# Optimization experiments

Measured on AMD Instinct MI355X. Metric: run time of the kernel, lower is better.

## Reference

```python
import jax, jax.numpy as jnp
import numpy as np

N = 100000   # nodes
E = 1600000  # edges (avg degree 16)
K = 50       # TAGConv hops per layer


def gcn_norm(edge_index, edge_weight, num_nodes):
    # PyG gcn_norm with add_self_loops=False: D^{-1/2} A D^{-1/2},
    # degree computed at the aggregation (col) side for source_to_target flow.
    row, col = edge_index[0], edge_index[1]
    deg = jax.ops.segment_sum(edge_weight, col, num_segments=num_nodes)
    dis = jnp.where(deg > 0, deg ** -0.5, jnp.zeros_like(deg))
    return dis[row] * edge_weight * dis[col]


def tagconv(x, row, col, norm, W, b):
    # out = sum_{k=0..K} (A_hat^k x) W_k + b, W: [K+1, fin, fout]
    out0 = x @ W[0] + b

    def step(carry, Wk):
        h, acc = carry
        h = jax.ops.segment_sum(norm[:, None] * h[row], col, num_segments=N)
        return (h, acc + h @ Wk), None

    (_, out), _ = jax.lax.scan(step, (x, out0), W[1:])
    return out


def setup_inputs() -> dict:
    key = jax.random.key(0)
    ks = jax.random.split(key, 8)
    edge_index = jax.random.randint(ks[0], (2, E), 0, N)
    edge_weight = jax.random.uniform(ks[1], (E,), dtype=jnp.float32)
    c = jax.random.normal(ks[2], (N,), dtype=jnp.float32)

    def glorot(k, fin, fout):
        lim = (6.0 / (fin + fout)) ** 0.5
        return jax.random.uniform(k, (K + 1, fin, fout), jnp.float32, -lim, lim)

    W1 = glorot(ks[3], 2, 15);  b1 = jnp.zeros((15,), jnp.float32)
    W2 = glorot(ks[4], 15, 30); b2 = jnp.zeros((30,), jnp.float32)
    W3 = glorot(ks[5], 30, 15); b3 = jnp.zeros((15,), jnp.float32)
    W4 = glorot(ks[6], 15, 1);  b4 = jnp.zeros((1,), jnp.float32)
    return {"edge_index": edge_index, "edge_weight": edge_weight, "c": c, "i": 123,
            "W1": W1, "b1": b1, "W2": W2, "b2": b2,
            "W3": W3, "b3": b3, "W4": W4, "b4": b4}


def reference(edge_index, edge_weight, c, i, W1, b1, W2, b2, W3, b3, W4, b4):
    cv = jnp.zeros((N,), jnp.float32).at[i].set(1.0)
    x = jnp.stack([cv, c], axis=1)  # [N, 2]
    row, col = edge_index[0], edge_index[1]
    norm = gcn_norm(edge_index, edge_weight.astype(jnp.float32), N)
    x = jax.nn.relu(tagconv(x, row, col, norm, W1, b1))
    x = jax.nn.relu(tagconv(x, row, col, norm, W2, b2))
    x = jax.nn.relu(tagconv(x, row, col, norm, W3, b3))
    x = jax.nn.relu(tagconv(x, row, col, norm, W4, b4))
    return jnp.squeeze(x)  # [N]
```

## Files before the change

### kernel.cpp

```cpp
#include <hip/hip_runtime.h>

#define NN 100000
#define NE 1600000
#define NB_N ((NN + 255) / 256)
#define NB_E ((NE + 255) / 256)
#define NB_G ((NN + 31) / 32)


__global__ void zero_kernel(int* __restrict__ cnt) {
    int i = blockIdx.x * 256 + threadIdx.x;
    if (i < NN) cnt[i] = 0;
}

__global__ void edge_pass1(const int* __restrict__ ei, int* __restrict__ cnt,
                           int* __restrict__ rank) {
    int e = blockIdx.x * 256 + threadIdx.x;
    if (e < NE) {
        int col = ei[NE + e];
        rank[e] = atomicAdd(&cnt[col], 1);
    }
}

__global__ void scan_block(const int* __restrict__ cnt, int* __restrict__ colptr,
                           int* __restrict__ bsum) {
    __shared__ int s[256];
    int t = threadIdx.x;
    int i = blockIdx.x * 256 + t;
    int v = (i < NN) ? cnt[i] : 0;
    s[t] = v;
    __syncthreads();
    for (int off = 1; off < 256; off <<= 1) {
        int x = (t >= off) ? s[t - off] : 0;
        __syncthreads();
        s[t] += x;
        __syncthreads();
    }
    if (i < NN) colptr[i] = s[t] - v;
    if (t == 255) bsum[blockIdx.x] = s[255];
}

__global__ void scan_top(int* __restrict__ bsum, int nb) {
    __shared__ int s[512];
    int t = threadIdx.x;
    int v = (t < nb) ? bsum[t] : 0;
    s[t] = v;
    __syncthreads();
    for (int off = 1; off < 512; off <<= 1) {
        int x = (t >= off) ? s[t - off] : 0;
        __syncthreads();
        s[t] += x;
        __syncthreads();
    }
    if (t < nb) bsum[t] = s[t] - v;
}

__global__ void scan_add(int* __restrict__ colptr, const int* __restrict__ bsum) {
    int i = blockIdx.x * 256 + threadIdx.x;
    if (i < NN) colptr[i] += bsum[blockIdx.x];
    if (i == 0) colptr[NN] = NE;
}

__global__ void scatter_kernel(const int* __restrict__ ei, const float* __restrict__ ew,
                               const int* __restrict__ colptr, const int* __restrict__ rank,
                               int2* __restrict__ pairs) {
    int e = blockIdx.x * 256 + threadIdx.x;
    if (e < NE) {
        int r = ei[e], col = ei[NE + e];
        pairs[colptr[col] + rank[e]] = make_int2(r, __float_as_int(ew[e]));
    }
}

__global__ void deg_dis_kernel(const int2* __restrict__ pairs, const int* __restrict__ colptr,
                               float* __restrict__ dis) {
    int n = blockIdx.x * 256 + threadIdx.x;
    if (n < NN) {
        int e0 = colptr[n], e1 = colptr[n + 1];
        float d = 0.f;
        for (int e = e0; e < e1; e++) d += __int_as_float(pairs[e].y);
        dis[n] = d > 0.f ? (float)(1.0 / sqrt((double)d)) : 0.f;
    }
}

__global__ void rescale_kernel(int2* __restrict__ pairs, const int* __restrict__ colptr,
                               const float* __restrict__ dis) {
    int n = blockIdx.x * 256 + threadIdx.x;
    if (n < NN) {
        float dn = dis[n];
        int e0 = colptr[n], e1 = colptr[n + 1];
        for (int e = e0; e < e1; e++) {
            int2 p = pairs[e];
            pairs[e] = make_int2(p.x, __float_as_int(dis[p.x] * __int_as_float(p.y) * dn));
        }
    }
}

__global__ void build_x(const float* __restrict__ c, const int* __restrict__ ip,
                        float2* __restrict__ X1) {
    int n = blockIdx.x * 256 + threadIdx.x;
    if (n < NN) {
        float2 v;
        v.x = (n == ip[0]) ? 1.f : 0.f;
        v.y = c[n];
        X1[n] = v;
    }
}


__launch_bounds__(256)
__global__ void init_acc1(const float2* __restrict__ X1, const float* __restrict__ W1,
                          const float* __restrict__ b1, float* __restrict__ acc) {
    __shared__ float sW[30], sb[15];
    int t = threadIdx.x;
    if (t < 30) sW[t] = W1[t];
    if (t < 15) sb[t] = b1[t];
    __syncthreads();
    int n = blockIdx.x * 256 + t;
    if (n >= NN) return;
    float2 x = X1[n];
    float a[16];
#pragma unroll
    for (int j = 0; j < 15; j++) a[j] = fmaf(x.x, sW[j], fmaf(x.y, sW[15 + j], sb[j]));
    a[15] = 0.f;
    float4* o = reinterpret_cast<float4*>(acc + (size_t)n * 16);
#pragma unroll
    for (int q = 0; q < 4; q++) o[q] = make_float4(a[4*q], a[4*q+1], a[4*q+2], a[4*q+3]);
}

__launch_bounds__(256)
__global__ void step1(const int2* __restrict__ pairs, const int* __restrict__ colptr,
                      const float2* __restrict__ hin, float2* __restrict__ hout,
                      float* __restrict__ acc, const float* __restrict__ Wk) {
    __shared__ float sW[32];
    int t = threadIdx.x;
    if (t < 32) {
        int f = t >> 4, j = t & 15;
        sW[t] = (j < 15) ? Wk[f * 15 + j] : 0.f;
    }
    __syncthreads();
    int g = t >> 3, l = t & 7;
    int n = blockIdx.x * 32 + g;
    if (n >= NN) return;
    int e0 = colptr[n], e1 = colptr[n + 1];
    float h0 = 0.f, h1 = 0.f;
    for (int e = e0 + l; e < e1; e += 8) {
        int2 p = pairs[e];
        float w = __int_as_float(p.y);
        float2 v = hin[p.x];
        h0 = fmaf(w, v.x, h0);
        h1 = fmaf(w, v.y, h1);
    }
    h0 += __shfl_xor(h0, 1); h1 += __shfl_xor(h1, 1);
    h0 += __shfl_xor(h0, 2); h1 += __shfl_xor(h1, 2);
    h0 += __shfl_xor(h0, 4); h1 += __shfl_xor(h1, 4);
    if (l == 0) hout[n] = make_float2(h0, h1);
    int j0 = 2 * l;
    float2* ap = reinterpret_cast<float2*>(acc + (size_t)n * 16 + j0);
    float2 a = *ap;
    a.x = fmaf(h0, sW[j0],     fmaf(h1, sW[16 + j0],     a.x));
    a.y = fmaf(h0, sW[j0 + 1], fmaf(h1, sW[16 + j0 + 1], a.y));
    *ap = a;
}

__global__ void relu1(const float* __restrict__ acc, float* __restrict__ X) {
    int n = blockIdx.x * 256 + threadIdx.x;
    if (n >= NN) return;
    const float4* ip = reinterpret_cast<const float4*>(acc + (size_t)n * 16);
    float4* op = reinterpret_cast<float4*>(X + (size_t)n * 16);
#pragma unroll
    for (int q = 0; q < 4; q++) {
        float4 v = ip[q];
        v.x = fmaxf(v.x, 0.f); v.y = fmaxf(v.y, 0.f);
        v.z = fmaxf(v.z, 0.f); v.w = fmaxf(v.w, 0.f);
        if (q == 3) v.w = 0.f;
        op[q] = v;
    }
}


__launch_bounds__(256)
__global__ void init_acc2(const float* __restrict__ X, const float* __restrict__ W2,
                          const float* __restrict__ b2, float4* __restrict__ acc) {
    __shared__ float sW[480];
    __shared__ float sb[32];
    int t = threadIdx.x;
    for (int q = t; q < 480; q += 256) {
        int f = q >> 5, j = q & 31;
        sW[q] = (j < 30) ? W2[f * 30 + j] : 0.f;
    }
    if (t < 32) sb[t] = (t < 30) ? b2[t] : 0.f;
    __syncthreads();
    int n = blockIdx.x * 256 + t;
    if (n >= NN) return;
    float h[15];
#pragma unroll
    for (int f = 0; f < 15; f++) h[f] = X[(size_t)n * 16 + f];
#pragma unroll
    for (int q = 0; q < 8; q++) {
        float4 a = make_float4(sb[4*q], sb[4*q+1], sb[4*q+2], sb[4*q+3]);
#pragma unroll
        for (int f = 0; f < 15; f++) {
            float hf = h[f];
            a.x = fmaf(hf, sW[f*32 + 4*q + 0], a.x);
            a.y = fmaf(hf, sW[f*32 + 4*q + 1], a.y);
            a.z = fmaf(hf, sW[f*32 + 4*q + 2], a.z);
            a.w = fmaf(hf, sW[f*32 + 4*q + 3], a.w);
        }
        acc[(size_t)n * 8 + q] = a;
    }
}

__launch_bounds__(256)
__global__ void step2(const int2* __restrict__ pairs, const int* __restrict__ colptr,
                      const float* __restrict__ hin, float* __restrict__ hout,
                      float4* __restrict__ acc, const float* __restrict__ Wk) {
    __shared__ float sW[480];
    __shared__ float sh[32][17];
    int t = threadIdx.x;
    for (int q = t; q < 480; q += 256) {
        int f = q >> 5, j = q & 31;
        sW[q] = (j < 30) ? Wk[f * 30 + j] : 0.f;
    }
    __syncthreads();
    int g = t >> 3, lane = t & 7;
    int n = blockIdx.x * 32 + g;
    if (n >= NN) return;
    float h0 = 0.f, h1 = 0.f;
    int e0 = colptr[n], e1 = colptr[n + 1];
    const float* hb = hin + 2 * lane;
    int e = e0;
    for (; e + 4 <= e1; e += 4) {
        int2 p0 = pairs[e + 0];
        int2 p1 = pairs[e + 1];
        int2 p2 = pairs[e + 2];
        int2 p3 = pairs[e + 3];
        float2 v0 = *reinterpret_cast<const float2*>(hb + (size_t)p0.x * 16);
        float2 v1 = *reinterpret_cast<const float2*>(hb + (size_t)p1.x * 16);
        float2 v2 = *reinterpret_cast<const float2*>(hb + (size_t)p2.x * 16);
        float2 v3 = *reinterpret_cast<const float2*>(hb + (size_t)p3.x * 16);
        float w0 = __int_as_float(p0.y), w1 = __int_as_float(p1.y);
        float w2 = __int_as_float(p2.y), w3 = __int_as_float(p3.y);
        h0 = fmaf(w0, v0.x, h0); h1 = fmaf(w0, v0.y, h1);
        h0 = fmaf(w1, v1.x, h0); h1 = fmaf(w1, v1.y, h1);
        h0 = fmaf(w2, v2.x, h0); h1 = fmaf(w2, v2.y, h1);
        h0 = fmaf(w3, v3.x, h0); h1 = fmaf(w3, v3.y, h1);
    }
    for (; e < e1; e++) {
        int2 p = pairs[e];
        float w = __int_as_float(p.y);
        float2 v = *reinterpret_cast<const float2*>(hb + (size_t)p.x * 16);
        h0 = fmaf(w, v.x, h0);
        h1 = fmaf(w, v.y, h1);
    }
    *reinterpret_cast<float2*>(hout + (size_t)n * 16 + 2 * lane) = make_float2(h0, h1);
    sh[g][2 * lane] = h0;
    sh[g][2 * lane + 1] = h1;
    __builtin_amdgcn_wave_barrier();
    float4 a = acc[(size_t)n * 8 + lane];
#pragma unroll
    for (int f = 0; f < 15; f++) {
        float hf = sh[g][f];
        a.x = fmaf(hf, sW[f*32 + 4*lane + 0], a.x);
        a.y = fmaf(hf, sW[f*32 + 4*lane + 1], a.y);
        a.z = fmaf(hf, sW[f*32 + 4*lane + 2], a.z);
        a.w = fmaf(hf, sW[f*32 + 4*lane + 3], a.w);
    }
    acc[(size_t)n * 8 + lane] = a;
}

__global__ void relu2(const float4* __restrict__ acc, float4* __restrict__ X3) {
    int n = blockIdx.x * 256 + threadIdx.x;
    if (n >= NN) return;
#pragma unroll
    for (int q = 0; q < 8; q++) {
        float4 v = acc[(size_t)n * 8 + q];
        v.x = fmaxf(v.x, 0.f); v.y = fmaxf(v.y, 0.f);
        v.z = fmaxf(v.z, 0.f); v.w = fmaxf(v.w, 0.f);
        if (q == 7) { v.z = 0.f; v.w = 0.f; }
        X3[(size_t)n * 8 + q] = v;
    }
}


__launch_bounds__(256)
__global__ void init3(const float* __restrict__ X3, const float* __restrict__ Wk,
                      float* __restrict__ rout) {
    __shared__ float sW[480];
    int t = threadIdx.x;
    for (int q = t; q < 480; q += 256) {
        int f = q >> 4, j = q & 15;
        sW[q] = (j < 15) ? Wk[f * 15 + j] : 0.f;
    }
    __syncthreads();
    int n = blockIdx.x * 256 + t;
    if (n >= NN) return;
    float h[30];
#pragma unroll
    for (int f = 0; f < 30; f++) h[f] = X3[(size_t)n * 32 + f];
    float z[16];
#pragma unroll
    for (int j = 0; j < 16; j++) z[j] = 0.f;
#pragma unroll
    for (int f = 0; f < 30; f++) {
        float hf = h[f];
#pragma unroll
        for (int j = 0; j < 15; j++) z[j] = fmaf(hf, sW[f*16 + j], z[j]);
    }
    float4* o = reinterpret_cast<float4*>(rout + (size_t)n * 16);
#pragma unroll
    for (int q = 0; q < 4; q++) o[q] = make_float4(z[4*q], z[4*q+1], z[4*q+2], z[4*q+3]);
}

__launch_bounds__(256)
__global__ void step3(const int2* __restrict__ pairs, const int* __restrict__ colptr,
                      const float* __restrict__ rin, float* __restrict__ rout,
                      const float* __restrict__ h0g, const float* __restrict__ Wk) {
    __shared__ float sW[480];
    __shared__ float sh[32][33];
    int t = threadIdx.x;
    for (int q = t; q < 480; q += 256) {
        int f = q >> 4, j = q & 15;
        sW[q] = (j < 15) ? Wk[f * 15 + j] : 0.f;
    }
    __syncthreads();
    int g = t >> 3, lane = t & 7;
    int n = blockIdx.x * 32 + g;
    if (n >= NN) return;
    float4 hv = *reinterpret_cast<const float4*>(h0g + (size_t)n * 32 + 4 * lane);
    sh[g][4*lane + 0] = hv.x; sh[g][4*lane + 1] = hv.y;
    sh[g][4*lane + 2] = hv.z; sh[g][4*lane + 3] = hv.w;
    __builtin_amdgcn_wave_barrier();
    int j0 = 2 * lane;
    float z0 = 0.f, z1 = 0.f;
#pragma unroll
    for (int f = 0; f < 30; f++) {
        float hf = sh[g][f];
        z0 = fmaf(hf, sW[f*16 + j0], z0);
        z1 = fmaf(hf, sW[f*16 + j0 + 1], z1);
    }
    int e0 = colptr[n], e1 = colptr[n + 1];
    const float* rb = rin + j0;
    int e = e0;
    for (; e + 4 <= e1; e += 4) {
        int2 p0 = pairs[e + 0];
        int2 p1 = pairs[e + 1];
        int2 p2 = pairs[e + 2];
        int2 p3 = pairs[e + 3];
        float2 v0 = *reinterpret_cast<const float2*>(rb + (size_t)p0.x * 16);
        float2 v1 = *reinterpret_cast<const float2*>(rb + (size_t)p1.x * 16);
        float2 v2 = *reinterpret_cast<const float2*>(rb + (size_t)p2.x * 16);
        float2 v3 = *reinterpret_cast<const float2*>(rb + (size_t)p3.x * 16);
        float w0 = __int_as_float(p0.y), w1 = __int_as_float(p1.y);
        float w2 = __int_as_float(p2.y), w3 = __int_as_float(p3.y);
        z0 = fmaf(w0, v0.x, z0); z1 = fmaf(w0, v0.y, z1);
        z0 = fmaf(w1, v1.x, z0); z1 = fmaf(w1, v1.y, z1);
        z0 = fmaf(w2, v2.x, z0); z1 = fmaf(w2, v2.y, z1);
        z0 = fmaf(w3, v3.x, z0); z1 = fmaf(w3, v3.y, z1);
    }
    for (; e < e1; e++) {
        int2 p = pairs[e];
        float w = __int_as_float(p.y);
        float2 v = *reinterpret_cast<const float2*>(rb + (size_t)p.x * 16);
        z0 = fmaf(w, v.x, z0);
        z1 = fmaf(w, v.y, z1);
    }
    *reinterpret_cast<float2*>(rout + (size_t)n * 16 + j0) = make_float2(z0, z1);
}

__global__ void relu3(const float* __restrict__ r, const float* __restrict__ b3,
                      float* __restrict__ X4) {
    __shared__ float sb[16];
    int t = threadIdx.x;
    if (t < 16) sb[t] = (t < 15) ? b3[t] : 0.f;
    __syncthreads();
    int n = blockIdx.x * 256 + t;
    if (n >= NN) return;
#pragma unroll
    for (int j = 0; j < 16; j++) {
        float v = (j < 15) ? fmaxf(r[(size_t)n * 16 + j] + sb[j], 0.f) : 0.f;
        X4[(size_t)n * 16 + j] = v;
    }
}


__launch_bounds__(256)
__global__ void init4(const float* __restrict__ X4, const float* __restrict__ Wk,
                      float* __restrict__ rout) {
    __shared__ float sW[16];
    int t = threadIdx.x;
    if (t < 16) sW[t] = (t < 15) ? Wk[t] : 0.f;
    __syncthreads();
    int n = blockIdx.x * 256 + t;
    if (n >= NN) return;
    float z = 0.f;
#pragma unroll
    for (int f = 0; f < 15; f++) z = fmaf(X4[(size_t)n * 16 + f], sW[f], z);
    rout[n] = z;
}

__launch_bounds__(256)
__global__ void step4(const int2* __restrict__ pairs, const int* __restrict__ colptr,
                      const float* __restrict__ rin, float* __restrict__ rout,
                      const float* __restrict__ h0g, const float* __restrict__ Wk) {
    __shared__ float sW[16];
    int t = threadIdx.x;
    if (t < 16) sW[t] = (t < 15) ? Wk[t] : 0.f;
    __syncthreads();
    int g = t >> 3, l = t & 7;
    int n = blockIdx.x * 32 + g;
    if (n >= NN) return;
    int j0 = 2 * l;
    float2 xv = *reinterpret_cast<const float2*>(h0g + (size_t)n * 16 + j0);
    float z = fmaf(xv.x, sW[j0], xv.y * sW[j0 + 1]);
    int e0 = colptr[n], e1 = colptr[n + 1];
    for (int e = e0 + l; e < e1; e += 8) {
        int2 p = pairs[e];
        z = fmaf(__int_as_float(p.y), rin[p.x], z);
    }
    z += __shfl_xor(z, 1);
    z += __shfl_xor(z, 2);
    z += __shfl_xor(z, 4);
    if (l == 0) rout[n] = z;
}

__global__ void out4(const float* __restrict__ r, const float* __restrict__ b4,
                     float* __restrict__ out) {
    int n = blockIdx.x * 256 + threadIdx.x;
    if (n < NN) out[n] = fmaxf(r[n] + b4[0], 0.f);
}


extern "C" void kernel_launch(void* const* d_in, const int* in_sizes, int n_in,
                              void* d_out, int out_size, void* d_ws, size_t ws_size,
                              hipStream_t stream) {
    const int*   ei = (const int*)d_in[0];
    const float* ew = (const float*)d_in[1];
    const float* c  = (const float*)d_in[2];
    const int*   ip = (const int*)d_in[3];
    const float* W1 = (const float*)d_in[4];  const float* b1 = (const float*)d_in[5];
    const float* W2 = (const float*)d_in[6];  const float* b2 = (const float*)d_in[7];
    const float* W3 = (const float*)d_in[8];  const float* b3 = (const float*)d_in[9];
    const float* W4 = (const float*)d_in[10]; const float* b4 = (const float*)d_in[11];
    float* out = (float*)d_out;

    char* ws = (char*)d_ws;
    size_t off = 0;
    auto alloc = [&](size_t bytes) -> char* {
        char* p = ws + off;
        off = (off + bytes + 255) & ~(size_t)255;
        return p;
    };
    int2*  pairs  = (int2*)alloc((size_t)NE * 8);
    int*   colptr = (int*)alloc((size_t)(NN + 1) * 4);
    int*   bsum   = (int*)alloc(512 * 4);
    float* HA     = (float*)alloc((size_t)NN * 16 * 4);
    float* HB     = (float*)alloc((size_t)NN * 16 * 4);
    char*  accR   = alloc((size_t)NN * 32 * 4);
    char*  x3R    = alloc((size_t)NN * 32 * 4);
    char*  x4R    = alloc((size_t)NN * 16 * 4);

    float*  ACC = (float*)accR;
    float*  RA  = (float*)accR;
    float*  RB  = (float*)(accR + (size_t)NN * 4);
    float*  X3  = (float*)x3R;
    int*    rank = (int*)x3R;
    int*    cnt  = (int*)(x3R + (size_t)NE * 4);
    float*  dis  = (float*)(x3R + (size_t)NE * 4 + (size_t)NN * 4);
    float*  X4  = (float*)x4R;
    float2* X1  = (float2*)x4R;

    zero_kernel<<<NB_N, 256, 0, stream>>>(cnt);
    edge_pass1<<<NB_E, 256, 0, stream>>>(ei, cnt, rank);
    scan_block<<<NB_N, 256, 0, stream>>>(cnt, colptr, bsum);
    scan_top<<<1, 512, 0, stream>>>(bsum, NB_N);
    scan_add<<<NB_N, 256, 0, stream>>>(colptr, bsum);
    scatter_kernel<<<NB_E, 256, 0, stream>>>(ei, ew, colptr, rank, pairs);
    deg_dis_kernel<<<NB_N, 256, 0, stream>>>(pairs, colptr, dis);
    rescale_kernel<<<NB_N, 256, 0, stream>>>(pairs, colptr, dis);
    build_x<<<NB_N, 256, 0, stream>>>(c, ip, X1);

    init_acc1<<<NB_N, 256, 0, stream>>>(X1, W1, b1, ACC);
    {
        const float2* hin = X1;
        float2* hout = (float2*)HA;
        for (int k = 1; k <= 50; k++) {
            step1<<<NB_G, 256, 0, stream>>>(pairs, colptr, hin, hout, ACC, W1 + (size_t)k * 30);
            hin = hout;
            hout = (hout == (float2*)HA) ? (float2*)HB : (float2*)HA;
        }
    }
    relu1<<<NB_N, 256, 0, stream>>>(ACC, HA);

    init_acc2<<<NB_N, 256, 0, stream>>>(HA, W2, b2, (float4*)ACC);
    {
        const float* hin = HA;
        float* hout = HB;
        for (int k = 1; k <= 50; k++) {
            step2<<<NB_G, 256, 0, stream>>>(pairs, colptr, hin, hout, (float4*)ACC,
                                            W2 + (size_t)k * 450);
            const float* tp = hin; hin = hout; hout = (float*)tp;
        }
    }
    relu2<<<NB_N, 256, 0, stream>>>((const float4*)ACC, (float4*)X3);

    init3<<<NB_N, 256, 0, stream>>>(X3, W3 + (size_t)50 * 450, HA);
    {
        const float* rin = HA;
        float* rout = HB;
        for (int k = 49; k >= 0; k--) {
            step3<<<NB_G, 256, 0, stream>>>(pairs, colptr, rin, rout, X3, W3 + (size_t)k * 450);
            const float* tp = rin; rin = rout; rout = (float*)tp;
        }
        relu3<<<NB_N, 256, 0, stream>>>(rin, b3, X4);
    }

    init4<<<NB_N, 256, 0, stream>>>(X4, W4 + (size_t)50 * 15, RA);
    {
        const float* rin = RA;
        float* rout = RB;
        for (int k = 49; k >= 0; k--) {
            step4<<<NB_G, 256, 0, stream>>>(pairs, colptr, rin, rout, X4, W4 + (size_t)k * 15);
            const float* tp = rin; rin = rout; rout = (float*)tp;
        }
        out4<<<NB_N, 256, 0, stream>>>(rin, b4, out);
    }
}
```

Before: 4.162 ms.

## Batch accumulator updates every two hops and use nontemporal edge-pair loads

Splits the layer-1 and layer-2 hop kernels into a propagate-only variant and a variant that propagates and then applies two hops' weights (the previous hop read from hin plus the current one) to the accumulator. This halves the read-modify-write traffic on the accumulator array across the 50-hop loops. Edge-pair loads in all propagation kernels become nontemporal loads, so the streamed CSR data is less likely to evict the gathered feature rows from cache. In exchange, the accumulating kernel reads hin[n] once more per node and uses twice the shared memory for weights.

```diff
diff --git a/kernel.cpp b/kernel.cpp
--- a/kernel.cpp
+++ b/kernel.cpp
@@ -5,6 +5,13 @@
 #define NB_N ((NN + 255) / 256)
 #define NB_E ((NE + 255) / 256)
 #define NB_G ((NN + 31) / 32)
+
+__device__ __forceinline__ void nt_pair(const int2* p, int& src, float& w) {
+    unsigned long long v = __builtin_nontemporal_load(
+        reinterpret_cast<const unsigned long long*>(p));
+    src = (int)(v & 0xffffffffull);
+    w = __int_as_float((int)(v >> 32));
+}
 
 
 __global__ void zero_kernel(int* __restrict__ cnt) {
@@ -127,25 +134,18 @@
 }
 
 __launch_bounds__(256)
-__global__ void step1(const int2* __restrict__ pairs, const int* __restrict__ colptr,
-                      const float2* __restrict__ hin, float2* __restrict__ hout,
-                      float* __restrict__ acc, const float* __restrict__ Wk) {
-    __shared__ float sW[32];
-    int t = threadIdx.x;
-    if (t < 32) {
-        int f = t >> 4, j = t & 15;
-        sW[t] = (j < 15) ? Wk[f * 15 + j] : 0.f;
-    }
-    __syncthreads();
+__global__ void step1_prop(const int2* __restrict__ pairs, const int* __restrict__ colptr,
+                           const float2* __restrict__ hin, float2* __restrict__ hout) {
+    int t = threadIdx.x;
     int g = t >> 3, l = t & 7;
     int n = blockIdx.x * 32 + g;
     if (n >= NN) return;
     int e0 = colptr[n], e1 = colptr[n + 1];
     float h0 = 0.f, h1 = 0.f;
     for (int e = e0 + l; e < e1; e += 8) {
-        int2 p = pairs[e];
-        float w = __int_as_float(p.y);
-        float2 v = hin[p.x];
+        int src; float w;
+        nt_pair(&pairs[e], src, w);
+        float2 v = hin[src];
         h0 = fmaf(w, v.x, h0);
         h1 = fmaf(w, v.y, h1);
     }
@@ -153,11 +153,44 @@
     h0 += __shfl_xor(h0, 2); h1 += __shfl_xor(h1, 2);
     h0 += __shfl_xor(h0, 4); h1 += __shfl_xor(h1, 4);
     if (l == 0) hout[n] = make_float2(h0, h1);
+}
+
+__launch_bounds__(256)
+__global__ void step1_acc(const int2* __restrict__ pairs, const int* __restrict__ colptr,
+                          const float2* __restrict__ hin, float2* __restrict__ hout,
+                          float* __restrict__ acc, const float* __restrict__ Wpair) {
+    __shared__ float sWm[32], sWk[32];
+    int t = threadIdx.x;
+    if (t < 32) {
+        int f = t >> 4, j = t & 15;
+        sWm[t] = (j < 15) ? Wpair[f * 15 + j] : 0.f;
+        sWk[t] = (j < 15) ? Wpair[30 + f * 15 + j] : 0.f;
+    }
+    __syncthreads();
+    int g = t >> 3, l = t & 7;
+    int n = blockIdx.x * 32 + g;
+    if (n >= NN) return;
+    int e0 = colptr[n], e1 = colptr[n + 1];
+    float h0 = 0.f, h1 = 0.f;
+    for (int e = e0 + l; e < e1; e += 8) {
+        int src; float w;
+        nt_pair(&pairs[e], src, w);
+        float2 v = hin[src];
+        h0 = fmaf(w, v.x, h0);
+        h1 = fmaf(w, v.y, h1);
+    }
+    h0 += __shfl_xor(h0, 1); h1 += __shfl_xor(h1, 1);
+    h0 += __shfl_xor(h0, 2); h1 += __shfl_xor(h1, 2);
+    h0 += __shfl_xor(h0, 4); h1 += __shfl_xor(h1, 4);
+    if (l == 0) hout[n] = make_float2(h0, h1);
+    float2 hm = hin[n];
     int j0 = 2 * l;
     float2* ap = reinterpret_cast<float2*>(acc + (size_t)n * 16 + j0);
     float2 a = *ap;
-    a.x = fmaf(h0, sW[j0],     fmaf(h1, sW[16 + j0],     a.x));
-    a.y = fmaf(h0, sW[j0 + 1], fmaf(h1, sW[16 + j0 + 1], a.y));
+    a.x = fmaf(h0, sWk[j0],     fmaf(h1, sWk[16 + j0],     a.x));
+    a.y = fmaf(h0, sWk[j0 + 1], fmaf(h1, sWk[16 + j0 + 1], a.y));
+    a.x = fmaf(hm.x, sWm[j0],     fmaf(hm.y, sWm[16 + j0],     a.x));
+    a.y = fmaf(hm.x, sWm[j0 + 1], fmaf(hm.y, sWm[16 + j0 + 1], a.y));
     *ap = a;
 }
 
@@ -210,17 +243,9 @@
 }
 
 __launch_bounds__(256)
-__global__ void step2(const int2* __restrict__ pairs, const int* __restrict__ colptr,
-                      const float* __restrict__ hin, float* __restrict__ hout,
-                      float4* __restrict__ acc, const float* __restrict__ Wk) {
-    __shared__ float sW[480];
-    __shared__ float sh[32][17];
-    int t = threadIdx.x;
-    for (int q = t; q < 480; q += 256) {
-        int f = q >> 5, j = q & 31;
-        sW[q] = (j < 30) ? Wk[f * 30 + j] : 0.f;
-    }
-    __syncthreads();
+__global__ void step2_prop(const int2* __restrict__ pairs, const int* __restrict__ colptr,
+                           const float* __restrict__ hin, float* __restrict__ hout) {
+    int t = threadIdx.x;
     int g = t >> 3, lane = t & 7;
     int n = blockIdx.x * 32 + g;
     if (n >= NN) return;
@@ -229,40 +254,86 @@
     const float* hb = hin + 2 * lane;
     int e = e0;
     for (; e + 4 <= e1; e += 4) {
-        int2 p0 = pairs[e + 0];
-        int2 p1 = pairs[e + 1];
-        int2 p2 = pairs[e + 2];
-        int2 p3 = pairs[e + 3];
-        float2 v0 = *reinterpret_cast<const float2*>(hb + (size_t)p0.x * 16);
-        float2 v1 = *reinterpret_cast<const float2*>(hb + (size_t)p1.x * 16);
-        float2 v2 = *reinterpret_cast<const float2*>(hb + (size_t)p2.x * 16);
-        float2 v3 = *reinterpret_cast<const float2*>(hb + (size_t)p3.x * 16);
-        float w0 = __int_as_float(p0.y), w1 = __int_as_float(p1.y);
-        float w2 = __int_as_float(p2.y), w3 = __int_as_float(p3.y);
+        int s0, s1, s2, s3; float w0, w1, w2, w3;
+        nt_pair(&pairs[e + 0], s0, w0);
+        nt_pair(&pairs[e + 1], s1, w1);
+        nt_pair(&pairs[e + 2], s2, w2);
+        nt_pair(&pairs[e + 3], s3, w3);
+        float2 v0 = *reinterpret_cast<const float2*>(hb + (size_t)s0 * 16);
+        float2 v1 = *reinterpret_cast<const float2*>(hb + (size_t)s1 * 16);
+        float2 v2 = *reinterpret_cast<const float2*>(hb + (size_t)s2 * 16);
+        float2 v3 = *reinterpret_cast<const float2*>(hb + (size_t)s3 * 16);
         h0 = fmaf(w0, v0.x, h0); h1 = fmaf(w0, v0.y, h1);
         h0 = fmaf(w1, v1.x, h0); h1 = fmaf(w1, v1.y, h1);
         h0 = fmaf(w2, v2.x, h0); h1 = fmaf(w2, v2.y, h1);
         h0 = fmaf(w3, v3.x, h0); h1 = fmaf(w3, v3.y, h1);
     }
     for (; e < e1; e++) {
-        int2 p = pairs[e];
-        float w = __int_as_float(p.y);
-        float2 v = *reinterpret_cast<const float2*>(hb + (size_t)p.x * 16);
+        int s; float w;
+        nt_pair(&pairs[e], s, w);
+        float2 v = *reinterpret_cast<const float2*>(hb + (size_t)s * 16);
         h0 = fmaf(w, v.x, h0);
         h1 = fmaf(w, v.y, h1);
     }
     *reinterpret_cast<float2*>(hout + (size_t)n * 16 + 2 * lane) = make_float2(h0, h1);
-    sh[g][2 * lane] = h0;
-    sh[g][2 * lane + 1] = h1;
+}
+
+__launch_bounds__(256)
+__global__ void step2_acc(const int2* __restrict__ pairs, const int* __restrict__ colptr,
+                          const float* __restrict__ hin, float* __restrict__ hout,
+                          float4* __restrict__ acc, const float* __restrict__ Wpair) {
+    __shared__ float sWm[480], sWk[480];
+    __shared__ float shm[32][17], shk[32][17];
+    int t = threadIdx.x;
+    for (int q = t; q < 480; q += 256) {
+        int f = q >> 5, j = q & 31;
+        sWm[q] = (j < 30) ? Wpair[f * 30 + j] : 0.f;
+        sWk[q] = (j < 30) ? Wpair[450 + f * 30 + j] : 0.f;
+    }
+    __syncthreads();
+    int g = t >> 3, lane = t & 7;
+    int n = blockIdx.x * 32 + g;
+    if (n >= NN) return;
+    float h0 = 0.f, h1 = 0.f;
+    int e0 = colptr[n], e1 = colptr[n + 1];
+    const float* hb = hin + 2 * lane;
+    int e = e0;
+    for (; e + 4 <= e1; e += 4) {
+        int s0, s1, s2, s3; float w0, w1, w2, w3;
+        nt_pair(&pairs[e + 0], s0, w0);
+        nt_pair(&pairs[e + 1], s1, w1);
+        nt_pair(&pairs[e + 2], s2, w2);
+        nt_pair(&pairs[e + 3], s3, w3);
+        float2 v0 = *reinterpret_cast<const float2*>(hb + (size_t)s0 * 16);
+        float2 v1 = *reinterpret_cast<const float2*>(hb + (size_t)s1 * 16);
+        float2 v2 = *reinterpret_cast<const float2*>(hb + (size_t)s2 * 16);
+        float2 v3 = *reinterpret_cast<const float2*>(hb + (size_t)s3 * 16);
+        h0 = fmaf(w0, v0.x, h0); h1 = fmaf(w0, v0.y, h1);
+        h0 = fmaf(w1, v1.x, h0); h1 = fmaf(w1, v1.y, h1);
+        h0 = fmaf(w2, v2.x, h0); h1 = fmaf(w2, v2.y, h1);
+        h0 = fmaf(w3, v3.x, h0); h1 = fmaf(w3, v3.y, h1);
+    }
+    for (; e < e1; e++) {
+        int s; float w;
+        nt_pair(&pairs[e], s, w);
+        float2 v = *reinterpret_cast<const float2*>(hb + (size_t)s * 16);
+        h0 = fmaf(w, v.x, h0);
+        h1 = fmaf(w, v.y, h1);
+    }
+    *reinterpret_cast<float2*>(hout + (size_t)n * 16 + 2 * lane) = make_float2(h0, h1);
+    float2 hm = *reinterpret_cast<const float2*>(hin + (size_t)n * 16 + 2 * lane);
+    shk[g][2 * lane] = h0;  shk[g][2 * lane + 1] = h1;
+    shm[g][2 * lane] = hm.x; shm[g][2 * lane + 1] = hm.y;
     __builtin_amdgcn_wave_barrier();
     float4 a = acc[(size_t)n * 8 + lane];
 #pragma unroll
     for (int f = 0; f < 15; f++) {
-        float hf = sh[g][f];
-        a.x = fmaf(hf, sW[f*32 + 4*lane + 0], a.x);
-        a.y = fmaf(hf, sW[f*32 + 4*lane + 1], a.y);
-        a.z = fmaf(hf, sW[f*32 + 4*lane + 2], a.z);
-        a.w = fmaf(hf, sW[f*32 + 4*lane + 3], a.w);
+        float hk = shk[g][f];
+        float hmf = shm[g][f];
+        a.x = fmaf(hk, sWk[f*32 + 4*lane + 0], fmaf(hmf, sWm[f*32 + 4*lane + 0], a.x));
+        a.y = fmaf(hk, sWk[f*32 + 4*lane + 1], fmaf(hmf, sWm[f*32 + 4*lane + 1], a.y));
+        a.z = fmaf(hk, sWk[f*32 + 4*lane + 2], fmaf(hmf, sWm[f*32 + 4*lane + 2], a.z));
+        a.w = fmaf(hk, sWk[f*32 + 4*lane + 3], fmaf(hmf, sWm[f*32 + 4*lane + 3], a.w));
     }
     acc[(size_t)n * 8 + lane] = a;
 }
@@ -341,25 +412,24 @@
     const float* rb = rin + j0;
     int e = e0;
     for (; e + 4 <= e1; e += 4) {
-        int2 p0 = pairs[e + 0];
-        int2 p1 = pairs[e + 1];
-        int2 p2 = pairs[e + 2];
-        int2 p3 = pairs[e + 3];
-        float2 v0 = *reinterpret_cast<const float2*>(rb + (size_t)p0.x * 16);
-        float2 v1 = *reinterpret_cast<const float2*>(rb + (size_t)p1.x * 16);
-        float2 v2 = *reinterpret_cast<const float2*>(rb + (size_t)p2.x * 16);
-        float2 v3 = *reinterpret_cast<const float2*>(rb + (size_t)p3.x * 16);
-        float w0 = __int_as_float(p0.y), w1 = __int_as_float(p1.y);
-        float w2 = __int_as_float(p2.y), w3 = __int_as_float(p3.y);
+        int s0, s1, s2, s3; float w0, w1, w2, w3;
+        nt_pair(&pairs[e + 0], s0, w0);
+        nt_pair(&pairs[e + 1], s1, w1);
+        nt_pair(&pairs[e + 2], s2, w2);
+        nt_pair(&pairs[e + 3], s3, w3);
+        float2 v0 = *reinterpret_cast<const float2*>(rb + (size_t)s0 * 16);
+        float2 v1 = *reinterpret_cast<const float2*>(rb + (size_t)s1 * 16);
+        float2 v2 = *reinterpret_cast<const float2*>(rb + (size_t)s2 * 16);
+        float2 v3 = *reinterpret_cast<const float2*>(rb + (size_t)s3 * 16);
         z0 = fmaf(w0, v0.x, z0); z1 = fmaf(w0, v0.y, z1);
         z0 = fmaf(w1, v1.x, z0); z1 = fmaf(w1, v1.y, z1);
         z0 = fmaf(w2, v2.x, z0); z1 = fmaf(w2, v2.y, z1);
         z0 = fmaf(w3, v3.x, z0); z1 = fmaf(w3, v3.y, z1);
     }
     for (; e < e1; e++) {
-        int2 p = pairs[e];
-        float w = __int_as_float(p.y);
-        float2 v = *reinterpret_cast<const float2*>(rb + (size_t)p.x * 16);
+        int s; float w;
+        nt_pair(&pairs[e], s, w);
+        float2 v = *reinterpret_cast<const float2*>(rb + (size_t)s * 16);
         z0 = fmaf(w, v.x, z0);
         z1 = fmaf(w, v.y, z1);
     }
@@ -413,8 +483,9 @@
     float z = fmaf(xv.x, sW[j0], xv.y * sW[j0 + 1]);
     int e0 = colptr[n], e1 = colptr[n + 1];
     for (int e = e0 + l; e < e1; e += 8) {
-        int2 p = pairs[e];
-        z = fmaf(__int_as_float(p.y), rin[p.x], z);
+        int s; float w;
+        nt_pair(&pairs[e], s, w);
+        z = fmaf(w, rin[s], z);
     }
     z += __shfl_xor(z, 1);
     z += __shfl_xor(z, 2);
@@ -483,7 +554,12 @@
         const float2* hin = X1;
         float2* hout = (float2*)HA;
         for (int k = 1; k <= 50; k++) {
-            step1<<<NB_G, 256, 0, stream>>>(pairs, colptr, hin, hout, ACC, W1 + (size_t)k * 30);
+            if (k & 1) {
+                step1_prop<<<NB_G, 256, 0, stream>>>(pairs, colptr, hin, hout);
+            } else {
+                step1_acc<<<NB_G, 256, 0, stream>>>(pairs, colptr, hin, hout, ACC,
+                                                    W1 + (size_t)(k - 1) * 30);
+            }
             hin = hout;
             hout = (hout == (float2*)HA) ? (float2*)HB : (float2*)HA;
         }
@@ -495,8 +571,12 @@
         const float* hin = HA;
         float* hout = HB;
         for (int k = 1; k <= 50; k++) {
-            step2<<<NB_G, 256, 0, stream>>>(pairs, colptr, hin, hout, (float4*)ACC,
-                                            W2 + (size_t)k * 450);
+            if (k & 1) {
+                step2_prop<<<NB_G, 256, 0, stream>>>(pairs, colptr, hin, hout);
+            } else {
+                step2_acc<<<NB_G, 256, 0, stream>>>(pairs, colptr, hin, hout, (float4*)ACC,
+                                                    W2 + (size_t)(k - 1) * 450);
+            }
             const float* tp = hin; hin = hout; hout = (float*)tp;
         }
     }
```

After: 5.153 ms. 1.24x slower.
